# Kernel tuning notes

Hardware: AMD Instinct MI355X
Metric: run time of the kernel (lower is better)

The kernel has to match this reference:

```python
import jax, jax.numpy as jnp
import numpy as np

B, L, D, DF, E, R = 4, 1024, 1024, 4096, 32768, 64
EPS = 1e-6


def layer_norm(x, g, b, eps=EPS):
    mu = x.mean(-1, keepdims=True)
    var = ((x - mu) ** 2).mean(-1, keepdims=True)
    return (x - mu) * jax.lax.rsqrt(var + eps) * g + b


def setup_inputs() -> dict:
    key = jax.random.key(0)
    ks = jax.random.split(key, 16)
    s = 0.02
    return {
        "hidden_states": jax.random.normal(ks[0], (B, L, D), jnp.float32),
        "rel_table": jax.random.normal(ks[1], (R, D), jnp.float32) * s,
        "Wq": jax.random.normal(ks[2], (D, D), jnp.float32) * s,
        "bq": jnp.zeros((D,), jnp.float32),
        "Wk": jax.random.normal(ks[3], (D, D), jnp.float32) * s,
        "Wv": jax.random.normal(ks[4], (D, D), jnp.float32) * s,
        "Wo": jax.random.normal(ks[5], (D, D), jnp.float32) * s,
        "bo": jnp.zeros((D,), jnp.float32),
        "ln0_g": jnp.ones((D,), jnp.float32),
        "ln0_b": jnp.zeros((D,), jnp.float32),
        "ln1_g": jnp.ones((D,), jnp.float32),
        "ln1_b": jnp.zeros((D,), jnp.float32),
        "W1": jax.random.normal(ks[6], (D, DF), jnp.float32) * s,
        "b1": jnp.zeros((DF,), jnp.float32),
        "W2": jax.random.normal(ks[7], (DF, D), jnp.float32) * s,
        "b2": jnp.zeros((D,), jnp.float32),
        "ln2_g": jnp.ones((D,), jnp.float32),
        "ln2_b": jnp.zeros((D,), jnp.float32),
        "edge_src": jax.random.randint(ks[8], (B, E), 0, L, jnp.int32),
        "edge_dst": jax.random.randint(ks[9], (B, E), 0, L, jnp.int32),
        "edge_rel": jax.random.randint(ks[10], (B, E), 0, R, jnp.int32),
    }


def reference(hidden_states, rel_table, Wq, bq, Wk, Wv, Wo, bo,
              ln0_g, ln0_b, ln1_g, ln1_b, W1, b1, W2, b2, ln2_g, ln2_b,
              edge_src, edge_dst, edge_rel):
    scale = np.sqrt(D).astype(np.float32)  # num_heads=1 -> d_k = D
    hs_norm = layer_norm(hidden_states, ln0_g, ln0_b)

    def rgat_one(x, src, dst, rel):
        # x: [L, D]; src/dst/rel: [E]
        e = rel_table[rel]                       # [E, D] relation embeddings
        q = x @ Wq + bq
        k = x @ Wk
        v = x @ Wv
        score = jnp.sum((k[src] + e) * q[dst], axis=-1) / scale      # [E]
        score = jnp.exp(jnp.clip(score, -10.0, 10.0))
        wv = jax.ops.segment_sum((v[src] + e) * score[:, None], dst, num_segments=L)
        z = jax.ops.segment_sum(score, dst, num_segments=L)          # [L]
        o = wv / z[:, None]
        out = layer_norm(x + o @ Wo + bo, ln1_g, ln1_b)
        ffn = jnp.maximum(out @ W1 + b1, 0.0) @ W2 + b2
        return layer_norm(out + ffn, ln2_g, ln2_b)

    graph_rep = jax.vmap(rgat_one)(hs_norm, edge_src, edge_dst, edge_rel)
    out = jax.nn.elu(graph_rep)                  # dropout = identity (eval)
    return hidden_states + out
```

## Files before the change

### kernel.cpp

```cpp
#include <hip/hip_runtime.h>
#include <hip/hip_bf16.h>

#define B_SZ 4
#define L_SEQ 1024
#define D_MODEL 1024
#define DF_FF 4096
#define E_PER_B 32768
#define R_REL 64
#define M_ROWS (B_SZ * L_SEQ)

typedef __attribute__((ext_vector_type(8))) short bf16x8;
typedef __attribute__((ext_vector_type(4))) float f32x4;

__device__ inline float b2f(unsigned short u) {
    union { unsigned int i; float f; } x; x.i = ((unsigned int)u) << 16; return x.f;
}
__device__ inline unsigned short f2b(float f) {
    union { float f; unsigned int u; } x; x.f = f;
    unsigned int r = x.u + 0x7FFFu + ((x.u >> 16) & 1u);
    return (unsigned short)(r >> 16);
}

#define GLOBAL_CAST(p) ((const __attribute__((address_space(1))) void*)(p))
#define LDS_CAST(p)    ((__attribute__((address_space(3))) void*)(p))

#define BT_QKV (1024u * 3072u)
#define SEXT_M 1152
#define LDA_WV 1088
#define LDB_WVP 1152
#define BT_WVP (1024u * 1152u)

__global__ void prep_all(const float* __restrict__ Wq, const float* __restrict__ Wk,
                         const float* __restrict__ Wv, const float* __restrict__ Wo,
                         const float* __restrict__ W1, const float* __restrict__ W2,
                         const float* __restrict__ rel, const float* __restrict__ bq,
                         const float* __restrict__ hidden,
                         const float* __restrict__ ln0_g, const float* __restrict__ ln0_b,
                         unsigned short* __restrict__ Wqkv_t, unsigned short* __restrict__ Wo_t,
                         unsigned short* __restrict__ W1_t, unsigned short* __restrict__ W2_t,
                         unsigned short* __restrict__ relbPad,
                         float* __restrict__ bqkv,
                         unsigned short* __restrict__ Xn_b16,
                         float* __restrict__ zeroReg) {
    __shared__ float tile[32][33];
    __shared__ float sb1[4], sb2[4];
    const int id = blockIdx.x, tid = threadIdx.x;
    if (id < 12288) {
        const float* src; unsigned short* dst; int K, N, x, y;
        if (id < 4096) {
            const int seg = id >> 10, t = id & 1023;
            K = 1024; N = 1024; x = t & 31; y = t >> 5;
            src = (seg == 0) ? Wq : (seg == 1) ? Wk : (seg == 2) ? Wv : Wo;
            dst = (seg == 3) ? Wo_t : (Wqkv_t + (size_t)seg * 1048576);
        } else if (id < 8192) {
            const int t = id - 4096; K = 1024; N = 4096; x = t & 127; y = t >> 7;
            src = W1; dst = W1_t;
        } else {
            const int t = id - 8192; K = 4096; N = 1024; x = t & 31; y = t >> 5;
            src = W2; dst = W2_t;
        }
        const int n0 = x * 32, k0 = y * 32, tx = tid & 31, ty = tid >> 5;
#pragma unroll
        for (int r = 0; r < 32; r += 8)
            tile[ty + r][tx] = src[(size_t)(k0 + ty + r) * N + (n0 + tx)];
        __syncthreads();
#pragma unroll
        for (int r = 0; r < 32; r += 8)
            dst[(size_t)(n0 + ty + r) * K + (k0 + tx)] = f2b(tile[tx][ty + r]);
    } else if (id < 12800) {
        const int i = (id - 12288) * 256 + tid;
        relbPad[i] = (i < 65536) ? f2b(rel[i]) : (unsigned short)0;
    } else if (id < 12812) {
        const int i = (id - 12800) * 256 + tid;
        bqkv[i] = (i < 1024) ? bq[i] : 0.0f;
    } else if (id < 16908) {
        const int row = id - 12812, t = tid;
        const size_t base = (size_t)row * 1024 + t * 4;
        float4 xv = *(const float4*)(hidden + base);
        float x0 = xv.x, x1 = xv.y, x2 = xv.z, x3 = xv.w;
        float s = x0 + x1 + x2 + x3;
#pragma unroll
        for (int o = 32; o > 0; o >>= 1) s += __shfl_down(s, o);
        if ((t & 63) == 0) sb1[t >> 6] = s;
        __syncthreads();
        const float mu = (sb1[0] + sb1[1] + sb1[2] + sb1[3]) * (1.0f / 1024.0f);
        const float d0 = x0 - mu, d1 = x1 - mu, d2 = x2 - mu, d3 = x3 - mu;
        float s2 = d0 * d0 + d1 * d1 + d2 * d2 + d3 * d3;
#pragma unroll
        for (int o = 32; o > 0; o >>= 1) s2 += __shfl_down(s2, o);
        if ((t & 63) == 0) sb2[t >> 6] = s2;
        __syncthreads();
        const float var = (sb2[0] + sb2[1] + sb2[2] + sb2[3]) * (1.0f / 1024.0f);
        const float rstd = rsqrtf(var + 1e-6f);
        const float4 gv = *(const float4*)(ln0_g + t * 4);
        const float4 bv = *(const float4*)(ln0_b + t * 4);
        ushort4 ob;
        ob.x = f2b(d0 * rstd * gv.x + bv.x);
        ob.y = f2b(d1 * rstd * gv.y + bv.y);
        ob.z = f2b(d2 * rstd * gv.z + bv.z);
        ob.w = f2b(d3 * rstd * gv.w + bv.w);
        *(ushort4*)(Xn_b16 + base) = ob;
    } else {
        const size_t base = (size_t)(id - 16908) * 4096 + tid * 4;
        const float4 z4 = make_float4(0.f, 0.f, 0.f, 0.f);
#pragma unroll
        for (int j = 0; j < 4; j++)
            *(float4*)(zeroReg + base + j * 1024) = z4;
    }
}

__device__ inline void tile_swizzle(int id, int ntn, int& tm, int& tn) {
    tm = ((id & 7) + ((id >> 3) / ntn) * 8) * 128;
    tn = ((id >> 3) % ntn) * 128;
}
__device__ inline void tsw256(int id, int ntn, int& tm, int& tn) {
    tm = ((id & 7) + ((id >> 3) / ntn) * 8) * 256;
    tn = ((id >> 3) % ntn) * 256;
}

#define GEMM_BODY(GA, LDA_, GB, LDB_, KLEN)                                                 \
    f32x4 acc[4][4];                                                                        \
    _Pragma("unroll") for (int i = 0; i < 4; i++)                                           \
        _Pragma("unroll") for (int j = 0; j < 4; j++) acc[i][j] = (f32x4)0.0f;              \
    for (int k0 = 0; k0 < (KLEN); k0 += 64) {                                               \
        __syncthreads();                                                                    \
        _Pragma("unroll") for (int r = 0; r < 4; ++r) {                                     \
            __builtin_amdgcn_global_load_lds(GLOBAL_CAST((GA) + (size_t)r * 8 * (LDA_)),    \
                LDS_CAST(&lA[(wave * 32 + r * 8) * 64]), 16, 0, 0);                         \
            __builtin_amdgcn_global_load_lds(GLOBAL_CAST((GB) + (size_t)r * 8 * (LDB_)),    \
                LDS_CAST(&lB[(wave * 32 + r * 8) * 64]), 16, 0, 0);                         \
        }                                                                                   \
        (GA) += 64; (GB) += 64;                                                             \
        __builtin_amdgcn_s_waitcnt(0);                                                      \
        __syncthreads();                                                                    \
        _Pragma("unroll") for (int kk = 0; kk < 2; ++kk) {                                  \
            const int cb = kk * 4 + quad;                                                   \
            bf16x8 af[4], bf[4];                                                            \
            _Pragma("unroll") for (int i = 0; i < 4; i++) {                                 \
                const int ra = wm + i * 16 + l16;                                           \
                af[i] = *(const bf16x8*)&lA[ra * 64 + ((cb ^ (ra & 7)) * 8)];               \
                const int rb = wn + i * 16 + l16;                                           \
                bf[i] = *(const bf16x8*)&lB[rb * 64 + ((cb ^ (rb & 7)) * 8)];               \
            }                                                                               \
            _Pragma("unroll") for (int mi = 0; mi < 4; mi++)                                \
                _Pragma("unroll") for (int ni = 0; ni < 4; ni++)                            \
                    acc[mi][ni] = __builtin_amdgcn_mfma_f32_16x16x32_bf16(                  \
                        af[mi], bf[ni], acc[mi][ni], 0, 0, 0);                              \
        }                                                                                   \
    }

#define ST_A(bufc, hh, kt) { \
    __builtin_amdgcn_global_load_lds(GLOBAL_CAST(gA[hh][0] + (kt) * 64), \
        LDS_CAST(&ls[bufc][0][((hh) * 128 + wv * 8) * 64]), 16, 0, 0); \
    __builtin_amdgcn_global_load_lds(GLOBAL_CAST(gA[hh][1] + (kt) * 64), \
        LDS_CAST(&ls[bufc][0][((hh) * 128 + 64 + wv * 8) * 64]), 16, 0, 0); }
#define ST_B(bufc, hh, kt) { \
    __builtin_amdgcn_global_load_lds(GLOBAL_CAST(gB[hh][0] + (kt) * 64), \
        LDS_CAST(&ls[bufc][1][((hh) * 128 + wv * 8) * 64]), 16, 0, 0); \
    __builtin_amdgcn_global_load_lds(GLOBAL_CAST(gB[hh][1] + (kt) * 64), \
        LDS_CAST(&ls[bufc][1][((hh) * 128 + 64 + wv * 8) * 64]), 16, 0, 0); }

#define PHASE(bufc, hh, gg, STMT, WAITSTMT) { \
    bf16x8 paf[4][2], pbf[2][2]; \
    _Pragma("unroll") for (int m4 = 0; m4 < 4; m4++) { \
        const int ra = ((hh) * 128 + wm * 64 + m4 * 16 + l16) * 64; \
        _Pragma("unroll") for (int kk = 0; kk < 2; kk++) \
            paf[m4][kk] = *(const bf16x8*)&ls[bufc][0][ra + (((kk * 4 + quad) ^ (l16 & 7)) * 8)]; \
    } \
    _Pragma("unroll") for (int ng = 0; ng < 2; ng++) { \
        const int rb2 = ((gg) * 128 + wc * 32 + ng * 16 + l16) * 64; \
        _Pragma("unroll") for (int kk = 0; kk < 2; kk++) \
            pbf[ng][kk] = *(const bf16x8*)&ls[bufc][1][rb2 + (((kk * 4 + quad) ^ (l16 & 7)) * 8)]; \
    } \
    STMT; \
    asm volatile("s_waitcnt lgkmcnt(8)"); \
    __builtin_amdgcn_s_barrier(); \
    asm volatile("s_waitcnt lgkmcnt(0)"); \
    __builtin_amdgcn_sched_barrier(0); \
    __builtin_amdgcn_s_setprio(1); \
    _Pragma("unroll") for (int m4 = 0; m4 < 4; m4++) \
        _Pragma("unroll") for (int ng = 0; ng < 2; ng++) \
            _Pragma("unroll") for (int kk = 0; kk < 2; kk++) \
                acc[(hh) * 4 + m4][(gg) * 2 + ng] = __builtin_amdgcn_mfma_f32_16x16x32_bf16( \
                    paf[m4][kk], pbf[ng][kk], acc[(hh) * 4 + m4][(gg) * 2 + ng], 0, 0, 0); \
    __builtin_amdgcn_s_setprio(0); \
    WAITSTMT; \
    __builtin_amdgcn_s_barrier(); }

template<bool RELU, bool SPLITK>
__global__ __launch_bounds__(512, 2)
void gemm256(const unsigned short* __restrict__ A, int lda,
             const unsigned short* __restrict__ Bt, int ldb,
             const float* __restrict__ bias,
             unsigned short* __restrict__ C, size_t pstride,
             int N, int Kc, int ntn) {
    __shared__ unsigned short ls[2][2][16384];
    int tile_m, tile_n;
    tsw256(blockIdx.x, ntn, tile_m, tile_n);
    const int t = threadIdx.x;
    const int wv = t >> 6, lane = t & 63;
    const int wm = wv >> 2;
    const int wc = wv & 3;
    const int quad = lane >> 4, l16 = lane & 15;
    const int srow8 = lane >> 3;
    const int schunk = ((lane & 7) ^ srow8) * 8;
    const int z = SPLITK ? blockIdx.z : 0;
    const int kofs = z * Kc;

    const unsigned short* gA[2][2];
    const unsigned short* gB[2][2];
#pragma unroll
    for (int h = 0; h < 2; h++)
#pragma unroll
        for (int j = 0; j < 2; j++) {
            const int rb = h * 2 + j;
            const int lb = ((rb & 1) << 1) | (rb >> 1);
            gA[h][j] = A + (size_t)(tile_m + lb * 64 + wv * 8 + srow8) * lda + kofs + schunk;
            const int nb = (j * 2 + (wv >> 2)) * 64 + h * 32 + (wv & 3) * 8;
            gB[h][j] = Bt + (size_t)(tile_n + nb + srow8) * ldb + kofs + schunk;
        }

    f32x4 acc[8][4];
#pragma unroll
    for (int i = 0; i < 8; i++)
#pragma unroll
        for (int j = 0; j < 4; j++) acc[i][j] = (f32x4)0.0f;

    ST_A(0, 0, 0); ST_B(0, 0, 0); ST_A(0, 1, 0); ST_B(0, 1, 0);
    ST_A(1, 0, 1); ST_B(1, 0, 1);
    asm volatile("s_waitcnt vmcnt(4)");
    __builtin_amdgcn_s_barrier();

    const int NI = Kc >> 7;
    for (int it = 0; it < NI - 1; ++it) {
        const int s1 = 2 * it + 1, s2 = 2 * it + 2, s3 = 2 * it + 3;
        PHASE(0, 0, 0, ST_A(1, 1, s1), );
        PHASE(0, 0, 1, ST_B(1, 1, s1), );
        PHASE(0, 1, 0, ST_A(0, 0, s2), );
        PHASE(0, 1, 1, ST_B(0, 0, s2), asm volatile("s_waitcnt vmcnt(4)"));
        PHASE(1, 0, 0, ST_A(0, 1, s2), );
        PHASE(1, 0, 1, ST_B(0, 1, s2), );
        PHASE(1, 1, 0, ST_A(1, 0, s3), );
        PHASE(1, 1, 1, ST_B(1, 0, s3), asm volatile("s_waitcnt vmcnt(4)"));
    }
    {
        const int sl = 2 * NI - 1;
        PHASE(0, 0, 0, ST_A(1, 1, sl), );
        PHASE(0, 0, 1, ST_B(1, 1, sl), );
        PHASE(0, 1, 0, , );
        PHASE(0, 1, 1, , asm volatile("s_waitcnt vmcnt(0)"));
        PHASE(1, 0, 0, , );
        PHASE(1, 0, 1, , );
        PHASE(1, 1, 0, , );
        PHASE(1, 1, 1, , );
    }

    unsigned short* Co = C + (SPLITK ? (size_t)z * pstride : 0);
#pragma unroll
    for (int mi = 0; mi < 8; mi++) {
#pragma unroll
        for (int ni = 0; ni < 4; ni++) {
            const int col = tile_n + wc * 64 + ni * 16 + l16;
            const float bv = (SPLITK && z != 0) ? 0.0f : bias[col];
#pragma unroll
            for (int r = 0; r < 4; r++) {
                const int row = tile_m + wm * 128 + mi * 16 + quad * 4 + r;
                float v = acc[mi][ni][r] + bv;
                if (RELU) v = fmaxf(v, 0.0f);
                Co[(size_t)row * N + col] = f2b(v);
            }
        }
    }
}

__global__ __launch_bounds__(256, 4)
void sext_w(const unsigned short* __restrict__ QKV,
            const unsigned short* __restrict__ relPad,
            const unsigned short* __restrict__ Wo_t,
            unsigned short* __restrict__ Pbase,
            unsigned short* __restrict__ Bwvp, int Kc) {
    __shared__ unsigned short lA[128 * 64];
    __shared__ unsigned short lB[128 * 64];
    const int id = blockIdx.x, t = threadIdx.x;
    const int wave = t >> 6, lane = t & 63;
    const int wm = (wave >> 1) * 64, wn = (wave & 1) * 64;
    const int quad = lane >> 4, l16 = lane & 15;
    const int srow = lane >> 3;
    const int schunk = ((lane & 7) ^ srow) * 8;

    if (id >= 576) {
        const int t2 = id - 576;
        const int b = t2 / 72, rem = t2 % 72;
        const int tile_m = (rem / 9) * 128;
        const int tile_n = (rem % 9) * 128;
        const unsigned short* gA = Wo_t + (size_t)(tile_m + wave * 32 + srow) * 1024 + schunk;
        const int brow = tile_n + wave * 32 + srow;
        const unsigned short* gB;
        size_t ldb;
        if (tile_n < 1024) {
            gB = QKV + (size_t)b * BT_QKV + (size_t)brow * 3072 + 2048 + schunk;
            ldb = 3072;
        } else {
            gB = relPad + (size_t)(brow - 1024) * 1024 + schunk;
            ldb = 1024;
        }
        GEMM_BODY(gA, 1024, gB, ldb, 1024)
        unsigned short* P = Bwvp + (size_t)b * BT_WVP;
#pragma unroll
        for (int mi = 0; mi < 4; mi++) {
#pragma unroll
            for (int ni = 0; ni < 4; ni++) {
                const int col = tile_n + wn + ni * 16 + l16;
#pragma unroll
                for (int r = 0; r < 4; r++) {
                    const int row = tile_m + wm + mi * 16 + quad * 4 + r;
                    P[(size_t)row * LDB_WVP + col] = f2b(acc[mi][ni][r]);
                }
            }
        }
        return;
    }

    const int bx = id % 72, b = (id / 72) & 3, z = id / 288;
    const int tile_m = (bx >> 3) * 128;
    const int tile_n = (bx & 7) * 128;
    const int kofs = z * Kc;
    const int arow = tile_m + wave * 32 + srow;
    const unsigned short* gA;
    size_t lda;
    if (tile_m < 1024) {
        gA = QKV + (size_t)b * BT_QKV + (size_t)arow * 3072 + 1024 + kofs + schunk;
        lda = 3072;
    } else {
        gA = relPad + (size_t)(arow - 1024) * 1024 + kofs + schunk;
        lda = 1024;
    }
    const unsigned short* gB = QKV + (size_t)b * BT_QKV
                                   + (size_t)(tile_n + wave * 32 + srow) * 3072 + kofs + schunk;
    GEMM_BODY(gA, lda, gB, 3072, Kc)
    unsigned short* P = Pbase + ((size_t)z * B_SZ + b) * (SEXT_M * 1024);
#pragma unroll
    for (int mi = 0; mi < 4; mi++) {
#pragma unroll
        for (int ni = 0; ni < 4; ni++) {
            const int col = tile_n + wn + ni * 16 + l16;
#pragma unroll
            for (int r = 0; r < 4; r++) {
                const int row = tile_m + wm + mi * 16 + quad * 4 + r;
                P[(size_t)row * 1024 + col] = f2b(acc[mi][ni][r]);
            }
        }
    }
}

__global__ __launch_bounds__(256, 4)
void gemm_wv_splitk(const unsigned short* __restrict__ A,
                    const unsigned short* __restrict__ Bt,
                    const float* __restrict__ bias,
                    unsigned short* __restrict__ Pbase, size_t pstride) {
    __shared__ unsigned short lA[128 * 64];
    __shared__ unsigned short lB[128 * 64];
    int tile_m, tile_n;
    tile_swizzle(blockIdx.x, 8, tile_m, tile_n);
    const int z = blockIdx.z;
    const int kofs = z * 576;
    const int Kc = z ? 512 : 576;
    const int t = threadIdx.x;
    const int wave = t >> 6, lane = t & 63;
    const int wm = (wave >> 1) * 64, wn = (wave & 1) * 64;
    const int quad = lane >> 4, l16 = lane & 15;
    const int srow = lane >> 3;
    const int schunk = ((lane & 7) ^ srow) * 8;
    const unsigned short* gA = A + (size_t)(tile_m + wave * 32 + srow) * LDA_WV + kofs + schunk;
    const unsigned short* gB = Bt + (size_t)(tile_m >> 10) * BT_WVP
                                  + (size_t)(tile_n + wave * 32 + srow) * LDB_WVP + kofs + schunk;
    GEMM_BODY(gA, LDA_WV, gB, LDB_WVP, Kc)
    unsigned short* P = Pbase + (size_t)z * pstride;
#pragma unroll
    for (int mi = 0; mi < 4; mi++) {
#pragma unroll
        for (int ni = 0; ni < 4; ni++) {
            const int col = tile_n + wn + ni * 16 + l16;
            const float bv = (z == 0) ? bias[col] : 0.0f;
#pragma unroll
            for (int r = 0; r < 4; r++) {
                const int row = tile_m + wm + mi * 16 + quad * 4 + r;
                P[(size_t)row * 1024 + col] = f2b(acc[mi][ni][r] + bv);
            }
        }
    }
}

template<bool FINAL, int NR>
__global__ void ln_kernel(const unsigned short* __restrict__ Xb,
                          const unsigned short* __restrict__ Rbase, size_t rstride,
                          const float* __restrict__ g, const float* __restrict__ be,
                          unsigned short* __restrict__ ob16,
                          const float* __restrict__ hidden, float* __restrict__ fout) {
    __shared__ float sb1[4], sb2[4];
    const int row = blockIdx.x, t = threadIdx.x;
    const size_t base = (size_t)row * 1024 + t * 4;

    ushort4 xv = *(const ushort4*)(Xb + base);
    float x0 = b2f(xv.x), x1 = b2f(xv.y), x2 = b2f(xv.z), x3 = b2f(xv.w);
#pragma unroll
    for (int r = 0; r < NR; r++) {
        ushort4 rv = *(const ushort4*)(Rbase + r * rstride + base);
        x0 += b2f(rv.x); x1 += b2f(rv.y); x2 += b2f(rv.z); x3 += b2f(rv.w);
    }
    float s = x0 + x1 + x2 + x3;
#pragma unroll
    for (int o = 32; o > 0; o >>= 1) s += __shfl_down(s, o);
    if ((t & 63) == 0) sb1[t >> 6] = s;
    __syncthreads();
    const float mu = (sb1[0] + sb1[1] + sb1[2] + sb1[3]) * (1.0f / 1024.0f);

    const float d0 = x0 - mu, d1 = x1 - mu, d2 = x2 - mu, d3 = x3 - mu;
    float s2 = d0 * d0 + d1 * d1 + d2 * d2 + d3 * d3;
#pragma unroll
    for (int o = 32; o > 0; o >>= 1) s2 += __shfl_down(s2, o);
    if ((t & 63) == 0) sb2[t >> 6] = s2;
    __syncthreads();
    const float var = (sb2[0] + sb2[1] + sb2[2] + sb2[3]) * (1.0f / 1024.0f);
    const float rstd = rsqrtf(var + 1e-6f);

    const float4 gv = *(const float4*)(g + t * 4);
    const float4 bv = *(const float4*)(be + t * 4);
    const float y0 = d0 * rstd * gv.x + bv.x;
    const float y1 = d1 * rstd * gv.y + bv.y;
    const float y2 = d2 * rstd * gv.z + bv.z;
    const float y3 = d3 * rstd * gv.w + bv.w;

    if (!FINAL) {
        ushort4 ob; ob.x = f2b(y0); ob.y = f2b(y1); ob.z = f2b(y2); ob.w = f2b(y3);
        *(ushort4*)(ob16 + base) = ob;
    } else {
        const float4 hv = *(const float4*)(hidden + base);
        const float e0 = y0 > 0.0f ? y0 : expm1f(y0);
        const float e1 = y1 > 0.0f ? y1 : expm1f(y1);
        const float e2 = y2 > 0.0f ? y2 : expm1f(y2);
        const float e3 = y3 > 0.0f ? y3 : expm1f(y3);
        float4 o; o.x = hv.x + e0; o.y = hv.y + e1; o.z = hv.z + e2; o.w = hv.w + e3;
        *(float4*)(fout + base) = o;
    }
}

__global__ void edge_scatter(const unsigned short* __restrict__ S,
                             const int* __restrict__ src, const int* __restrict__ dst,
                             const int* __restrict__ rel,
                             float* __restrict__ A, float* __restrict__ G) {
    const size_t ZSTR = (size_t)B_SZ * SEXT_M * 1024;
    const int gg = blockIdx.x * 256 + threadIdx.x;
    const int b = gg >> 15;
    const int s = src[gg], d = dst[gg], r = rel[gg];
    const size_t sbase = ((size_t)b * SEXT_M + s) * 1024 + d;
    const size_t tbase = ((size_t)b * SEXT_M + 1024 + r) * 1024 + d;
    const float sval = b2f(S[sbase]) + b2f(S[sbase + ZSTR]);
    const float tval = b2f(S[tbase]) + b2f(S[tbase + ZSTR]);
    float sc = (sval + tval) * (1.0f / 32.0f);
    sc = expf(fminf(fmaxf(sc, -10.0f), 10.0f));
    atomicAdd(&A[((size_t)((b << 10) + d) << 10) + s], sc);
    atomicAdd(&G[((size_t)((b << 10) + d) << 6) + r], sc);
}

__global__ void normalize(const float* __restrict__ A, const float* __restrict__ G,
                          unsigned short* __restrict__ Awv) {
    __shared__ float sInv;
    const int row = blockIdx.x, t = threadIdx.x;
    float v = 0.0f;
    if (t < 64) {
        v = G[(size_t)row * 64 + t];
        float s = v;
#pragma unroll
        for (int o = 1; o < 64; o <<= 1) s += __shfl_xor(s, o);
        if (t == 0) sInv = 1.0f / s;
    }
    __syncthreads();
    const float inv = sInv;
    const size_t obase = (size_t)row * LDA_WV;
    const float4 a = *(const float4*)(A + (size_t)row * 1024 + t * 4);
    ushort4 o;
    o.x = f2b(a.x * inv); o.y = f2b(a.y * inv); o.z = f2b(a.z * inv); o.w = f2b(a.w * inv);
    *(ushort4*)(Awv + obase + t * 4) = o;
    if (t < 16) {
        const float4 gq = *(const float4*)(G + (size_t)row * 64 + t * 4);
        ushort4 og;
        og.x = f2b(gq.x * inv); og.y = f2b(gq.y * inv);
        og.z = f2b(gq.z * inv); og.w = f2b(gq.w * inv);
        *(ushort4*)(Awv + obase + 1024 + t * 4) = og;
    }
}

extern "C" void kernel_launch(void* const* d_in, const int* in_sizes, int n_in,
                              void* d_out, int out_size, void* d_ws, size_t ws_size,
                              hipStream_t stream) {
    const float* hidden  = (const float*)d_in[0];
    const float* rel_tbl = (const float*)d_in[1];
    const float* Wq = (const float*)d_in[2];
    const float* bq = (const float*)d_in[3];
    const float* Wk = (const float*)d_in[4];
    const float* Wv = (const float*)d_in[5];
    const float* Wo = (const float*)d_in[6];
    const float* bo = (const float*)d_in[7];
    const float* ln0_g = (const float*)d_in[8];
    const float* ln0_b = (const float*)d_in[9];
    const float* ln1_g = (const float*)d_in[10];
    const float* ln1_b = (const float*)d_in[11];
    const float* W1 = (const float*)d_in[12];
    const float* b1 = (const float*)d_in[13];
    const float* W2 = (const float*)d_in[14];
    const float* b2 = (const float*)d_in[15];
    const float* ln2_g = (const float*)d_in[16];
    const float* ln2_b = (const float*)d_in[17];
    const int* esrc = (const int*)d_in[18];
    const int* edst = (const int*)d_in[19];
    const int* erel = (const int*)d_in[20];
    float* out = (float*)d_out;

    char* ws = (char*)d_ws;
    const size_t MB = 1024 * 1024;
    unsigned short* Xn_b16  = (unsigned short*)(ws + 16 * MB);
    unsigned short* H1      = (unsigned short*)(ws + 0);
    unsigned short* Wqkv_t  = (unsigned short*)(ws + 24 * MB);
    unsigned short* Wo_t    = (unsigned short*)(ws + 30 * MB);
    unsigned short* W1_t    = (unsigned short*)(ws + 32 * MB);
    unsigned short* W2_t    = (unsigned short*)(ws + 40 * MB);
    unsigned short* relbPad = (unsigned short*)(ws + 48 * MB);
    float*          bqkv    = (float*)(ws + 48 * MB + 512 * 1024);
    unsigned short* QKV     = (unsigned short*)(ws + 49 * MB);
    unsigned short* Awv     = (unsigned short*)(ws + 49 * MB);
    unsigned short* Qw2H    = (unsigned short*)(ws + 49 * MB);
    unsigned short* PwoH    = (unsigned short*)(ws + 66 * MB);
    unsigned short* SxH     = (unsigned short*)(ws + 73 * MB);
    unsigned short* Bwvp    = (unsigned short*)(ws + 92 * MB);
    float*          Amat    = (float*)(ws + 101 * MB);
    float*          Gmat    = (float*)(ws + 117 * MB);
    unsigned short* Out_b16 = (unsigned short*)(ws + 113 * MB);

    const size_t PSTRIDE_H = 4u * 1024 * 1024;
    const dim3 blk(256);
    const dim3 blk512(512);

    prep_all<<<17996, blk, 0, stream>>>(Wq, Wk, Wv, Wo, W1, W2, rel_tbl, bq,
                                        hidden, ln0_g, ln0_b,
                                        Wqkv_t, Wo_t, W1_t, W2_t, relbPad, bqkv,
                                        Xn_b16, Amat);
    gemm256<false, false><<<dim3(192), blk512, 0, stream>>>(
        Xn_b16, 1024, Wqkv_t, 1024, bqkv, QKV, 0, 3072, 1024, 12);
    sext_w<<<864, blk, 0, stream>>>(QKV, relbPad, Wo_t, SxH, Bwvp, 512);
    edge_scatter<<<512, blk, 0, stream>>>(SxH, esrc, edst, erel, Amat, Gmat);
    normalize<<<M_ROWS, blk, 0, stream>>>(Amat, Gmat, Awv);
    gemm_wv_splitk<<<dim3(256, 1, 2), blk, 0, stream>>>(Awv, Bwvp, bo, PwoH, PSTRIDE_H);
    ln_kernel<false, 2><<<M_ROWS, blk, 0, stream>>>(Xn_b16, PwoH, PSTRIDE_H, ln1_g, ln1_b,
                                                    Out_b16, nullptr, nullptr);
    gemm256<true, false><<<dim3(256), blk512, 0, stream>>>(
        Out_b16, 1024, W1_t, 1024, b1, H1, 0, 4096, 1024, 16);
    gemm256<false, true><<<dim3(64, 1, 4), blk512, 0, stream>>>(
        H1, 4096, W2_t, 4096, b2, Qw2H, PSTRIDE_H, 1024, 1024, 4);
    ln_kernel<true, 4><<<M_ROWS, blk, 0, stream>>>(Out_b16, Qw2H, PSTRIDE_H, ln2_g, ln2_b,
                                                   nullptr, hidden, out);
    (void)in_sizes; (void)n_in; (void)out_size; (void)ws_size;
}
```

Baseline: 360.2 us.

## Restructure 256-tile GEMM phases to split along K and reuse B fragments

The 8-phase pipelined bf16 GEMM now splits each 64-wide K tile into two 32-wide halves per phase. B fragments are loaded once every two phases and reused across both A row-halves. The global-to-LDS load order and row mapping are simplified to contiguous rows, and the mid-phase lgkmcnt/barrier pair before the MFMAs is removed. The aim is fewer LDS reads and barriers per MFMA, at the cost of a shorter prefetch distance (vmcnt(2)) and a changed write-after-read hazard pattern.

```diff
diff --git a/kernel.cpp b/kernel.cpp
--- a/kernel.cpp
+++ b/kernel.cpp
@@ -149,40 +149,35 @@
         }                                                                                   \
     }
 
-#define ST_A(bufc, hh, kt) { \
-    __builtin_amdgcn_global_load_lds(GLOBAL_CAST(gA[hh][0] + (kt) * 64), \
-        LDS_CAST(&ls[bufc][0][((hh) * 128 + wv * 8) * 64]), 16, 0, 0); \
-    __builtin_amdgcn_global_load_lds(GLOBAL_CAST(gA[hh][1] + (kt) * 64), \
-        LDS_CAST(&ls[bufc][0][((hh) * 128 + 64 + wv * 8) * 64]), 16, 0, 0); }
-#define ST_B(bufc, hh, kt) { \
-    __builtin_amdgcn_global_load_lds(GLOBAL_CAST(gB[hh][0] + (kt) * 64), \
-        LDS_CAST(&ls[bufc][1][((hh) * 128 + wv * 8) * 64]), 16, 0, 0); \
-    __builtin_amdgcn_global_load_lds(GLOBAL_CAST(gB[hh][1] + (kt) * 64), \
-        LDS_CAST(&ls[bufc][1][((hh) * 128 + 64 + wv * 8) * 64]), 16, 0, 0); }
-
-#define PHASE(bufc, hh, gg, STMT, WAITSTMT) { \
-    bf16x8 paf[4][2], pbf[2][2]; \
-    _Pragma("unroll") for (int m4 = 0; m4 < 4; m4++) { \
-        const int ra = ((hh) * 128 + wm * 64 + m4 * 16 + l16) * 64; \
-        _Pragma("unroll") for (int kk = 0; kk < 2; kk++) \
-            paf[m4][kk] = *(const bf16x8*)&ls[bufc][0][ra + (((kk * 4 + quad) ^ (l16 & 7)) * 8)]; \
+#define ST_A2(bufc, hh, kt) { \
+    _Pragma("unroll") for (int j = 0; j < 2; j++) \
+        __builtin_amdgcn_global_load_lds(GLOBAL_CAST(gA[hh][j] + (size_t)(kt) * 64), \
+            LDS_CAST(&ls[bufc][0][((hh) * 128 + j * 64 + wv * 8) * 64]), 16, 0, 0); }
+#define ST_B2(bufc, hh, kt) { \
+    _Pragma("unroll") for (int j = 0; j < 2; j++) \
+        __builtin_amdgcn_global_load_lds(GLOBAL_CAST(gB[hh][j] + (size_t)(kt) * 64), \
+            LDS_CAST(&ls[bufc][1][((hh) * 128 + j * 64 + wv * 8) * 64]), 16, 0, 0); }
+
+#define VM2 asm volatile("s_waitcnt vmcnt(2)" ::: "memory")
+#define VM0 asm volatile("s_waitcnt vmcnt(0)" ::: "memory")
+
+#define PHASE(bufc, hhw, kkc, RB, STMT, WAITSTMT) { \
+    STMT; \
+    const int slotx = ((((kkc) * 4) + quad) ^ (l16 & 7)) * 8; \
+    if (RB) { \
+        _Pragma("unroll") for (int ni = 0; ni < 4; ni++) \
+            pbf[ni] = *(const bf16x8*)&ls[bufc][1][(wc * 64 + ni * 16 + l16) * 64 + slotx]; \
     } \
-    _Pragma("unroll") for (int ng = 0; ng < 2; ng++) { \
-        const int rb2 = ((gg) * 128 + wc * 32 + ng * 16 + l16) * 64; \
-        _Pragma("unroll") for (int kk = 0; kk < 2; kk++) \
-            pbf[ng][kk] = *(const bf16x8*)&ls[bufc][1][rb2 + (((kk * 4 + quad) ^ (l16 & 7)) * 8)]; \
-    } \
-    STMT; \
-    asm volatile("s_waitcnt lgkmcnt(8)"); \
-    __builtin_amdgcn_s_barrier(); \
-    asm volatile("s_waitcnt lgkmcnt(0)"); \
+    bf16x8 paf[4]; \
+    _Pragma("unroll") for (int m4 = 0; m4 < 4; m4++) \
+        paf[m4] = *(const bf16x8*)&ls[bufc][0][(wm * 128 + (hhw) * 64 + m4 * 16 + l16) * 64 + slotx]; \
+    asm volatile("s_waitcnt lgkmcnt(0)" ::: "memory"); \
     __builtin_amdgcn_sched_barrier(0); \
     __builtin_amdgcn_s_setprio(1); \
     _Pragma("unroll") for (int m4 = 0; m4 < 4; m4++) \
-        _Pragma("unroll") for (int ng = 0; ng < 2; ng++) \
-            _Pragma("unroll") for (int kk = 0; kk < 2; kk++) \
-                acc[(hh) * 4 + m4][(gg) * 2 + ng] = __builtin_amdgcn_mfma_f32_16x16x32_bf16( \
-                    paf[m4][kk], pbf[ng][kk], acc[(hh) * 4 + m4][(gg) * 2 + ng], 0, 0, 0); \
+        _Pragma("unroll") for (int ni = 0; ni < 4; ni++) \
+            acc[(hhw) * 4 + m4][ni] = __builtin_amdgcn_mfma_f32_16x16x32_bf16( \
+                paf[m4], pbf[ni], acc[(hhw) * 4 + m4][ni], 0, 0, 0); \
     __builtin_amdgcn_s_setprio(0); \
     WAITSTMT; \
     __builtin_amdgcn_s_barrier(); }
@@ -213,11 +208,8 @@
     for (int h = 0; h < 2; h++)
 #pragma unroll
         for (int j = 0; j < 2; j++) {
-            const int rb = h * 2 + j;
-            const int lb = ((rb & 1) << 1) | (rb >> 1);
-            gA[h][j] = A + (size_t)(tile_m + lb * 64 + wv * 8 + srow8) * lda + kofs + schunk;
-            const int nb = (j * 2 + (wv >> 2)) * 64 + h * 32 + (wv & 3) * 8;
-            gB[h][j] = Bt + (size_t)(tile_n + nb + srow8) * ldb + kofs + schunk;
+            gA[h][j] = A + (size_t)(tile_m + h * 128 + j * 64 + wv * 8 + srow8) * lda + kofs + schunk;
+            gB[h][j] = Bt + (size_t)(tile_n + h * 128 + j * 64 + wv * 8 + srow8) * ldb + kofs + schunk;
         }
 
     f32x4 acc[8][4];
@@ -225,34 +217,35 @@
     for (int i = 0; i < 8; i++)
 #pragma unroll
         for (int j = 0; j < 4; j++) acc[i][j] = (f32x4)0.0f;
-
-    ST_A(0, 0, 0); ST_B(0, 0, 0); ST_A(0, 1, 0); ST_B(0, 1, 0);
-    ST_A(1, 0, 1); ST_B(1, 0, 1);
-    asm volatile("s_waitcnt vmcnt(4)");
+    bf16x8 pbf[4];
+
+    ST_A2(0, 0, 0); ST_A2(0, 1, 0); ST_B2(0, 0, 0); ST_B2(0, 1, 0);
+    ST_B2(1, 0, 1);
+    VM2;
     __builtin_amdgcn_s_barrier();
 
     const int NI = Kc >> 7;
     for (int it = 0; it < NI - 1; ++it) {
-        const int s1 = 2 * it + 1, s2 = 2 * it + 2, s3 = 2 * it + 3;
-        PHASE(0, 0, 0, ST_A(1, 1, s1), );
-        PHASE(0, 0, 1, ST_B(1, 1, s1), );
-        PHASE(0, 1, 0, ST_A(0, 0, s2), );
-        PHASE(0, 1, 1, ST_B(0, 0, s2), asm volatile("s_waitcnt vmcnt(4)"));
-        PHASE(1, 0, 0, ST_A(0, 1, s2), );
-        PHASE(1, 0, 1, ST_B(0, 1, s2), );
-        PHASE(1, 1, 0, ST_A(1, 0, s3), );
-        PHASE(1, 1, 1, ST_B(1, 0, s3), asm volatile("s_waitcnt vmcnt(4)"));
+        const int ks = 2 * it;
+        PHASE(0, 0, 0, 1, ST_A2(1, 0, ks + 1), )
+        PHASE(0, 1, 0, 0, ST_A2(1, 1, ks + 1), )
+        PHASE(0, 0, 1, 1, ST_B2(1, 1, ks + 1), )
+        PHASE(0, 1, 1, 0, ST_B2(0, 0, ks + 2), VM2)
+        PHASE(1, 0, 0, 1, ST_A2(0, 0, ks + 2), )
+        PHASE(1, 1, 0, 0, ST_A2(0, 1, ks + 2), )
+        PHASE(1, 0, 1, 1, ST_B2(0, 1, ks + 2), )
+        PHASE(1, 1, 1, 0, ST_B2(1, 0, ks + 3), VM2)
     }
     {
-        const int sl = 2 * NI - 1;
-        PHASE(0, 0, 0, ST_A(1, 1, sl), );
-        PHASE(0, 0, 1, ST_B(1, 1, sl), );
-        PHASE(0, 1, 0, , );
-        PHASE(0, 1, 1, , asm volatile("s_waitcnt vmcnt(0)"));
-        PHASE(1, 0, 0, , );
-        PHASE(1, 0, 1, , );
-        PHASE(1, 1, 0, , );
-        PHASE(1, 1, 1, , );
+        const int ks = 2 * (NI - 1);
+        PHASE(0, 0, 0, 1, ST_A2(1, 0, ks + 1), )
+        PHASE(0, 1, 0, 0, ST_A2(1, 1, ks + 1), )
+        PHASE(0, 0, 1, 1, ST_B2(1, 1, ks + 1), )
+        PHASE(0, 1, 1, 0, , VM0)
+        PHASE(1, 0, 0, 1, , )
+        PHASE(1, 1, 0, 0, , )
+        PHASE(1, 0, 1, 1, , )
+        PHASE(1, 1, 1, 0, , )
     }
 
     unsigned short* Co = C + (SPLITK ? (size_t)z * pstride : 0);
```

Measured after the change: 351.4 us. 2.4% less time.
